# Optimization experiments

Hardware: AMD Instinct MI355X
Metric: run time of the kernel (lower is better)

## Reference

```python
import jax, jax.numpy as jnp
import numpy as np

D_MODEL = 1024
HEAD = 16
K_D = D_MODEL // HEAD
SEQ_LEN = 2048
BATCH = 4
NEG = 1e10


def setup_inputs() -> dict:
    key = jax.random.key(0)
    ks = jax.random.split(key, 5)
    x = jax.random.normal(ks[0], (BATCH, SEQ_LEN, D_MODEL), dtype=jnp.float32)
    # params (torch Linear stored as [out,in]; we store [in,out] and matmul directly)
    W_attn = jax.random.normal(ks[1], (D_MODEL, 3 * D_MODEL), dtype=jnp.float32) * 0.02
    b_attn = jnp.zeros((3 * D_MODEL,), dtype=jnp.float32)
    W_proj = jax.random.normal(ks[2], (D_MODEL, D_MODEL), dtype=jnp.float32) * 0.02
    b_proj = jnp.zeros((D_MODEL,), dtype=jnp.float32)
    return {"x": x, "W_attn": W_attn, "b_attn": b_attn, "W_proj": W_proj, "b_proj": b_proj}


def reference(x, W_attn, b_attn, W_proj, b_proj):
    B, S, D = x.shape
    qkv = x @ W_attn + b_attn                     # [B,S,3D]
    # NOTE: source splits as (value, query, key) in that order
    value, query, key = jnp.split(qkv, 3, axis=-1)

    def heads(t):  # [B,S,D] -> [B,H,S,k_d]
        return t.reshape(B, S, HEAD, K_D).transpose(0, 2, 1, 3)

    v, q, k = heads(value), heads(query), heads(key)
    present = jnp.stack((k, v))                   # [2,B,H,S,k_d]

    scores = jnp.einsum('bhqd,bhkd->bhqk', q, k) / jnp.sqrt(jnp.float32(K_D))
    bias = jnp.tril(jnp.ones((S, S), dtype=scores.dtype))[None, None]
    scores = scores * bias - NEG * (1.0 - bias)
    attn = jax.nn.softmax(scores, axis=-1)
    out = jnp.einsum('bhqk,bhkd->bhqd', attn, v)  # [B,H,S,k_d]
    out = out.transpose(0, 2, 1, 3).reshape(B, S, D)
    out = out @ W_proj + b_proj
    return out, present
```

## Files before the change

### kernel.cpp

```cpp
#include <hip/hip_runtime.h>

typedef __attribute__((ext_vector_type(8))) short short8;
typedef __attribute__((ext_vector_type(4))) short short4v;
typedef __attribute__((ext_vector_type(4))) float f32x4;
typedef __attribute__((ext_vector_type(16))) float f32x16;
typedef __attribute__((ext_vector_type(4))) unsigned int u32x4;
typedef __attribute__((ext_vector_type(2))) unsigned int u32x2;
typedef unsigned int u32;

#define D_MODEL 1024
#define HEADS 16
#define KD 64
#define SEQ 2048
#define BATCH 4
#define NTOK (BATCH*SEQ)
#define QKV_N (3*D_MODEL)

__device__ inline float bf2f(unsigned short u) {
    unsigned x = ((unsigned)u) << 16;
    return __builtin_bit_cast(float, x);
}
__device__ inline unsigned short f2bf(float f) {
    unsigned u = __builtin_bit_cast(unsigned, f);
    u += 0x7FFFu + ((u >> 16) & 1u);
    return (unsigned short)(u >> 16);
}
__device__ __forceinline__ void gload_lds16(const unsigned short* g, unsigned short* l) {
    __builtin_amdgcn_global_load_lds(
        (const __attribute__((address_space(1))) void*)g,
        (__attribute__((address_space(3))) void*)l, 16, 0, 0);
}
__device__ __forceinline__ u32 cvtpk(float lo, float hi) {
    u32 r; asm("v_cvt_pk_bf16_f32 %0, %1, %2" : "=v"(r) : "v"(lo), "v"(hi)); return r;
}
__device__ __forceinline__ void pl32swap(u32& a, u32& b) {
#if __has_builtin(__builtin_amdgcn_permlane32_swap)
    u32x2 r = __builtin_amdgcn_permlane32_swap(a, b, 0, 0);
    a = r[0]; b = r[1];
#else
    u32 pa = (u32)__shfl_xor((int)a, 32, 64);
    u32 pb = (u32)__shfl_xor((int)b, 32, 64);
    bool hb = (threadIdx.x & 32) != 0;
    u32 na = hb ? pb : a;
    u32 nb = hb ? b : pa;
    a = na; b = nb;
#endif
}
__device__ __forceinline__ float pairmax(float x) {
    u32 a = __builtin_bit_cast(u32, x), b = a;
    pl32swap(a, b);
    return fmaxf(x, fmaxf(__builtin_bit_cast(float, a), __builtin_bit_cast(float, b)));
}
__device__ __forceinline__ float pairsum(float x) {
    u32 a = __builtin_bit_cast(u32, x), b = a;
    pl32swap(a, b);
    return __builtin_bit_cast(float, a) + __builtin_bit_cast(float, b);
}

__global__ __launch_bounds__(256) void cvt_kernel(
    const float* __restrict__ x, unsigned short* __restrict__ y)
{
    size_t i = (size_t)blockIdx.x * 256 + threadIdx.x;
    f32x4 a = *reinterpret_cast<const f32x4*>(x + i*8);
    f32x4 b = *reinterpret_cast<const f32x4*>(x + i*8 + 4);
    short8 o;
    #pragma unroll
    for (int j = 0; j < 4; ++j) { o[j] = (short)f2bf(a[j]); o[j+4] = (short)f2bf(b[j]); }
    *reinterpret_cast<short8*>(y + i*8) = o;
}

__global__ __launch_bounds__(256) void transpose_kernel(
    const float* __restrict__ W, unsigned short* __restrict__ WT, int K, int N)
{
    __shared__ unsigned short T[64][80];
    const int tid = threadIdx.x;
    const int n0 = blockIdx.x * 64, k0 = blockIdx.y * 64;

    int r  = tid >> 2;
    int cq = tid & 3;
    const float* src = W + (size_t)(k0 + r) * N + n0 + cq*16;
    #pragma unroll
    for (int q = 0; q < 4; ++q) {
        f32x4 v = *reinterpret_cast<const f32x4*>(src + q*4);
        #pragma unroll
        for (int j = 0; j < 4; ++j) T[cq*16 + q*4 + j][r] = f2bf(v[j]);
    }
    __syncthreads();
    int c  = tid >> 2;
    int rq = tid & 3;
    short8 o0 = *reinterpret_cast<const short8*>(&T[c][rq*16]);
    short8 o1 = *reinterpret_cast<const short8*>(&T[c][rq*16 + 8]);
    unsigned short* dst = WT + (size_t)(n0 + c) * K + k0 + rq*16;
    *reinterpret_cast<short8*>(dst)     = o0;
    *reinterpret_cast<short8*>(dst + 8) = o1;
}

template<int Y_F32, int FUSE>
__global__ __launch_bounds__(256) void gemm_bt_kernel(
    const unsigned short* __restrict__ A, const unsigned short* __restrict__ BT,
    const float* __restrict__ bias, void* __restrict__ Yv,
    unsigned short* __restrict__ vtg, float* __restrict__ pres,
    int M, int N, int K)
{
    __shared__ unsigned short sA[2][128*64];
    __shared__ unsigned short sB[2][128*64];

    const int tid = threadIdx.x, lane = tid & 63, w = tid >> 6;
    const int l15 = lane & 15, lg = lane >> 4;

    const int nwg = gridDim.x * gridDim.y;
    const int bid = blockIdx.y * gridDim.x + blockIdx.x;
    const int swz = (bid & 7) * (nwg >> 3) + (bid >> 3);
    const int n0 = (swz % gridDim.x) * 128;
    const int m0 = (swz / gridDim.x) * 128;

    const int wr = w >> 1, wc = w & 1;

    f32x4 acc[4][4];
    #pragma unroll
    for (int m = 0; m < 4; ++m)
        #pragma unroll
        for (int n = 0; n < 4; ++n) acc[m][n] = f32x4{0,0,0,0};

    const int ldrow = (lane >> 3);
    const int slot  = lane & 7;
    const int nkt = K >> 6;

    #pragma unroll
    for (int i = 0; i < 4; ++i) {
        int kb  = w*4 + i;
        int row = kb*8 + ldrow;
        int sc  = slot ^ (row & 7);
        gload_lds16(&A [(size_t)(m0 + row) * K + sc*8], &sA[0][kb*512]);
        gload_lds16(&BT[(size_t)(n0 + row) * K + sc*8], &sB[0][kb*512]);
    }
    __syncthreads();

    for (int kt = 0; kt < nkt; ++kt) {
        const int buf = kt & 1;

        if (kt + 1 < nkt) {
            const int k1 = (kt + 1) << 6;
            #pragma unroll
            for (int i = 0; i < 4; ++i) {
                int kb  = w*4 + i;
                int row = kb*8 + ldrow;
                int sc  = slot ^ (row & 7);
                gload_lds16(&A [(size_t)(m0 + row) * K + k1 + sc*8], &sA[buf^1][kb*512]);
                gload_lds16(&BT[(size_t)(n0 + row) * K + k1 + sc*8], &sB[buf^1][kb*512]);
            }
        }

        #pragma unroll
        for (int kk = 0; kk < 2; ++kk) {
            short8 af[4], bfr[4];
            #pragma unroll
            for (int m = 0; m < 4; ++m) {
                int row = wr*64 + m*16 + l15;
                int ch  = (4*kk + lg) ^ (row & 7);
                af[m] = *reinterpret_cast<const short8*>(&sA[buf][row*64 + ch*8]);
            }
            #pragma unroll
            for (int n = 0; n < 4; ++n) {
                int row = wc*64 + n*16 + l15;
                int ch  = (4*kk + lg) ^ (row & 7);
                bfr[n] = *reinterpret_cast<const short8*>(&sB[buf][row*64 + ch*8]);
            }
            __builtin_amdgcn_s_setprio(1);
            #pragma unroll
            for (int m = 0; m < 4; ++m)
                #pragma unroll
                for (int n = 0; n < 4; ++n)
                    acc[m][n] = __builtin_amdgcn_mfma_f32_16x16x32_bf16(
                        af[m], bfr[n], acc[m][n], 0, 0, 0);
            __builtin_amdgcn_s_setprio(0);
        }
        __syncthreads();
    }

    #pragma unroll
    for (int n = 0; n < 4; ++n) {
        int col = n0 + wc*64 + n*16 + l15;
        float bv = bias[col];
        #pragma unroll
        for (int m = 0; m < 4; ++m) {
            int row0 = m0 + wr*64 + m*16 + lg*4;
            float v0 = acc[m][n][0] + bv;
            float v1 = acc[m][n][1] + bv;
            float v2 = acc[m][n][2] + bv;
            float v3 = acc[m][n][3] + bv;
            if (Y_F32) {
                float* Y = (float*)Yv;
                Y[(size_t)(row0+0) * N + col] = v0;
                Y[(size_t)(row0+1) * N + col] = v1;
                Y[(size_t)(row0+2) * N + col] = v2;
                Y[(size_t)(row0+3) * N + col] = v3;
            } else {
                unsigned short* Y = (unsigned short*)Yv;
                Y[(size_t)(row0+0) * N + col] = f2bf(v0);
                Y[(size_t)(row0+1) * N + col] = f2bf(v1);
                Y[(size_t)(row0+2) * N + col] = f2bf(v2);
                Y[(size_t)(row0+3) * N + col] = f2bf(v3);
            }
            if (FUSE && n0 < D_MODEL) {
                int hh = col >> 6, dd = col & 63;
                int bb = row0 >> 11, ss = row0 & (SEQ - 1);
                short4v pk;
                pk[0] = (short)f2bf(v0); pk[1] = (short)f2bf(v1);
                pk[2] = (short)f2bf(v2); pk[3] = (short)f2bf(v3);
                *reinterpret_cast<short4v*>(
                    vtg + (((size_t)bb*HEADS + hh)*KD + dd)*SEQ + ss) = pk;
                float* pv = pres + (size_t)BATCH*HEADS*SEQ*KD
                          + (((size_t)bb*HEADS + hh)*SEQ + ss)*KD + dd;
                pv[0] = v0; pv[KD] = v1; pv[2*KD] = v2; pv[3*KD] = v3;
            }
            if (FUSE && n0 >= 2*D_MODEL) {
                int rel = col - 2*D_MODEL;
                int hh = rel >> 6, dd = rel & 63;
                int bb = row0 >> 11, ss = row0 & (SEQ - 1);
                float* pk2 = pres + (((size_t)bb*HEADS + hh)*SEQ + ss)*KD + dd;
                pk2[0] = v0; pk2[KD] = v1; pk2[2*KD] = v2; pk2[3*KD] = v3;
            }
        }
    }
}

__global__ __launch_bounds__(256) void attn_kernel(
    const unsigned short* __restrict__ qkv,
    const unsigned short* __restrict__ vtg,
    unsigned short* __restrict__ aout)
{
    __shared__ unsigned short Kl[2][64*64];
    __shared__ unsigned short Vl[2][64*64];

    const int tid  = threadIdx.x;
    const int lane = tid & 63;
    const int w    = tid >> 6;
    const int l31  = lane & 31, hi = lane >> 5;

    const int bid = blockIdx.x;
    const int hb  = bid & 63;
    const int qb  = 15 - (bid >> 6);
    const int h = hb & 15, b = hb >> 4;

    const unsigned short* base  = qkv + (size_t)b * SEQ * QKV_N;
    const unsigned short* vbase = vtg + ((size_t)b * HEADS + h) * KD * SEQ;
    const int qoff = D_MODEL + h*KD;
    const int koff = 2*D_MODEL + h*KD;

    const float SCALE2 = 0.125f * 1.44269504088896f;
    const float THR_RAW = 44.36f;

    const int ldrow = lane >> 3;
    const int slot  = lane & 7;
    const int ksw   = l31 & 7;

    const int q0 = qb * 128;
    const int qrow  = q0 + w*32 + l31;
    const int qminw = q0 + w*32;

    short8 qf[4];
    #pragma unroll
    for (int ks = 0; ks < 4; ++ks)
        qf[ks] = *reinterpret_cast<const short8*>(
            base + (size_t)qrow * QKV_N + qoff + ks*16 + hi*8);

    f32x16 o0, o1;
    #pragma unroll
    for (int r = 0; r < 16; ++r) { o0[r] = 0.f; o1[r] = 0.f; }
    float m = -1e30f, msc = -1e30f * 0.180336887f, sr = 0.f;

    const int nt = 2*qb + 2;

    #pragma unroll
    for (int i = 0; i < 2; ++i) {
        int kb = w*2 + i, row = kb*8 + ldrow, sc = slot ^ (row & 7);
        gload_lds16(&base[(size_t)row * QKV_N + koff + sc*8], &Kl[0][kb*512]);
        gload_lds16(&vbase[(size_t)row * SEQ + sc*8],         &Vl[0][kb*512]);
    }
    __syncthreads();

    for (int t = 0; t < nt; ++t) {
        const int buf = t & 1;

        if (t + 1 < nt) {
            #pragma unroll
            for (int i = 0; i < 2; ++i) {
                int kb = w*2 + i, row = kb*8 + ldrow, sc = slot ^ (row & 7);
                gload_lds16(&base[(size_t)((t+1)*64 + row) * QKV_N + koff + sc*8],
                            &Kl[buf^1][kb*512]);
                gload_lds16(&vbase[(size_t)row * SEQ + (t+1)*64 + sc*8],
                            &Vl[buf^1][kb*512]);
            }
        }

        const int d0 = qminw - t*64;
        if (d0 > -32) {
            f32x16 sa, sb;
            #pragma unroll
            for (int r = 0; r < 16; ++r) { sa[r] = 0.f; sb[r] = 0.f; }
            __builtin_amdgcn_s_setprio(1);
            #pragma unroll
            for (int ks = 0; ks < 4; ++ks) {
                short8 kf = *reinterpret_cast<const short8*>(
                    &Kl[buf][l31*64 + ((2*ks + hi) ^ ksw)*8]);
                sa = __builtin_amdgcn_mfma_f32_32x32x16_bf16(kf, qf[ks], sa, 0, 0, 0);
            }
            #pragma unroll
            for (int ks = 0; ks < 4; ++ks) {
                short8 kf = *reinterpret_cast<const short8*>(
                    &Kl[buf][(32 + l31)*64 + ((2*ks + hi) ^ ksw)*8]);
                sb = __builtin_amdgcn_mfma_f32_32x32x16_bf16(kf, qf[ks], sb, 0, 0, 0);
            }
            __builtin_amdgcn_s_setprio(0);

            if (d0 <= 32) {
                const int kqA = l31 + d0      - 4*hi;
                const int kqB = l31 + d0 - 32 - 4*hi;
                #pragma unroll
                for (int r = 0; r < 16; ++r) {
                    const int cr = (r & 3) + 8*(r >> 2);
                    if (d0 == 0) sa[r] = (cr <= kqA) ? sa[r] : -1e30f;
                    sb[r] = (cr <= kqB) ? sb[r] : -1e30f;
                }
            }

            float x[8];
            #pragma unroll
            for (int i = 0; i < 8; ++i)
                x[i] = fmaxf(fmaxf(sa[2*i], sa[2*i+1]), fmaxf(sb[2*i], sb[2*i+1]));
            float pm = fmaxf(fmaxf(fmaxf(x[0], x[1]), fmaxf(x[2], x[3])),
                             fmaxf(fmaxf(x[4], x[5]), fmaxf(x[6], x[7])));
            pm = pairmax(pm);
            if (!__all(pm <= m + THR_RAW)) {
                float mn  = fmaxf(m, pm);
                float fac = exp2f((m - mn) * SCALE2);
                sr *= fac;
                #pragma unroll
                for (int r = 0; r < 16; ++r) { o0[r] *= fac; o1[r] *= fac; }
                m = mn; msc = m * SCALE2;
            }

            #pragma unroll
            for (int r = 0; r < 16; ++r) {
                sa[r] = exp2f(sa[r]*SCALE2 - msc);
                sb[r] = exp2f(sb[r]*SCALE2 - msc);
            }
            float u[8];
            #pragma unroll
            for (int i = 0; i < 8; ++i)
                u[i] = (sa[2*i] + sa[2*i+1]) + (sb[2*i] + sb[2*i+1]);
            float ts = ((u[0]+u[1]) + (u[2]+u[3])) + ((u[4]+u[5]) + (u[6]+u[7]));
            sr += pairsum(ts);

            u32 WA[8], WB[8];
            #pragma unroll
            for (int wi = 0; wi < 8; ++wi) {
                WA[wi] = cvtpk(sa[2*wi], sa[2*wi+1]);
                WB[wi] = cvtpk(sb[2*wi], sb[2*wi+1]);
            }

            #pragma unroll
            for (int h32 = 0; h32 < 2; ++h32) {
                #pragma unroll
                for (int ks = 0; ks < 2; ++ks) {
                    u32 W0 = h32 ? WB[4*ks+0] : WA[4*ks+0];
                    u32 W1 = h32 ? WB[4*ks+1] : WA[4*ks+1];
                    u32 W2 = h32 ? WB[4*ks+2] : WA[4*ks+2];
                    u32 W3 = h32 ? WB[4*ks+3] : WA[4*ks+3];
                    u32 s0 = hi ? W0 : W2;
                    u32 s1 = hi ? W1 : W3;
                    u32 r0 = (u32)__shfl_xor((int)s0, 32, 64);
                    u32 r1 = (u32)__shfl_xor((int)s1, 32, 64);
                    u32x4 wv;
                    wv[0] = hi ? r0 : W0;
                    wv[1] = hi ? r1 : W1;
                    wv[2] = hi ? W2 : r0;
                    wv[3] = hi ? W3 : r1;
                    short8 pfrag = __builtin_bit_cast(short8, wv);
                    __builtin_amdgcn_s_setprio(1);
                    #pragma unroll
                    for (int dt = 0; dt < 2; ++dt) {
                        short8 vf = *reinterpret_cast<const short8*>(
                            &Vl[buf][(dt*32 + l31)*64 + ((4*h32 + 2*ks + hi) ^ ksw)*8]);
                        if (dt == 0)
                            o0 = __builtin_amdgcn_mfma_f32_32x32x16_bf16(vf, pfrag, o0, 0, 0, 0);
                        else
                            o1 = __builtin_amdgcn_mfma_f32_32x32x16_bf16(vf, pfrag, o1, 0, 0, 0);
                    }
                    __builtin_amdgcn_s_setprio(0);
                }
            }
        }
        __syncthreads();
    }

    const float inv = 1.0f / sr;
    unsigned short* orow = aout + ((size_t)b * SEQ + qrow) * D_MODEL + h*KD;
    #pragma unroll
    for (int dt = 0; dt < 2; ++dt) {
        #pragma unroll
        for (int g = 0; g < 4; ++g) {
            short4v pk;
            #pragma unroll
            for (int j = 0; j < 4; ++j) {
                float v = (dt == 0 ? o0[4*g + j] : o1[4*g + j]) * inv;
                pk[j] = (short)f2bf(v);
            }
            *reinterpret_cast<short4v*>(orow + dt*32 + 8*g + 4*hi) = pk;
        }
    }
}

extern "C" void kernel_launch(void* const* d_in, const int* in_sizes, int n_in,
                              void* d_out, int out_size, void* d_ws, size_t ws_size,
                              hipStream_t stream)
{
    const float* x      = (const float*)d_in[0];
    const float* W_attn = (const float*)d_in[1];
    const float* b_attn = (const float*)d_in[2];
    const float* W_proj = (const float*)d_in[3];
    const float* b_proj = (const float*)d_in[4];
    float* out = (float*)d_out;

    unsigned short* qkv  = (unsigned short*)d_ws;
    unsigned short* xbf  = qkv + (size_t)NTOK * QKV_N;
    unsigned short* aout = xbf;
    unsigned short* WT   = xbf + (size_t)NTOK * D_MODEL;
    unsigned short* WpT  = WT + (size_t)QKV_N * D_MODEL;
    unsigned short* vtg  = WpT + (size_t)D_MODEL * D_MODEL;
    float* pres = out + (size_t)NTOK * D_MODEL;

    cvt_kernel<<<(NTOK * D_MODEL / 8) / 256, 256, 0, stream>>>(x, xbf);
    dim3 gt1(QKV_N / 64, D_MODEL / 64);
    transpose_kernel<<<gt1, 256, 0, stream>>>(W_attn, WT, D_MODEL, QKV_N);
    dim3 gt2(D_MODEL / 64, D_MODEL / 64);
    transpose_kernel<<<gt2, 256, 0, stream>>>(W_proj, WpT, D_MODEL, D_MODEL);

    dim3 g1(QKV_N / 128, NTOK / 128);
    gemm_bt_kernel<0, 1><<<g1, 256, 0, stream>>>(xbf, WT, b_attn, qkv, vtg, pres,
                                                 NTOK, QKV_N, D_MODEL);

    attn_kernel<<<1024, 256, 0, stream>>>(qkv, vtg, aout);

    dim3 g2(D_MODEL / 128, NTOK / 128);
    gemm_bt_kernel<1, 0><<<g2, 256, 0, stream>>>(aout, WpT, b_proj, out,
                                                 nullptr, nullptr,
                                                 NTOK, D_MODEL, D_MODEL);
}
```

Baseline: 210.5 us.

## Pair complementary causal query blocks per workgroup to share K/V tiles

Each attention workgroup now processes two query blocks, p and 15-p, so every block does equal causal work, and the grid halves. The K/V tiles loaded into LDS are reused for both query blocks while their ranges overlap, which cuts global and LDS load traffic per unit of work. The code is split into qk/softmax/pv helpers. Doubled accumulator and Q-fragment state raises register pressure, which may reduce occupancy.

```diff
diff --git a/kernel.cpp b/kernel.cpp
--- a/kernel.cpp
+++ b/kernel.cpp
@@ -55,6 +55,117 @@
     u32 a = __builtin_bit_cast(u32, x), b = a;
     pl32swap(a, b);
     return __builtin_bit_cast(float, a) + __builtin_bit_cast(float, b);
+}
+
+#define SCALE2f (0.125f * 1.44269504088896f)
+#define THR_RAWf 44.36f
+
+__device__ __forceinline__ void qk_tile(
+    const unsigned short* __restrict__ Klb, const short8 (&qf)[4],
+    int l31, int hi, int ksw, f32x16& sa, f32x16& sb)
+{
+    #pragma unroll
+    for (int r = 0; r < 16; ++r) { sa[r] = 0.f; sb[r] = 0.f; }
+    __builtin_amdgcn_s_setprio(1);
+    #pragma unroll
+    for (int ks = 0; ks < 4; ++ks) {
+        short8 kf = *reinterpret_cast<const short8*>(
+            &Klb[l31*64 + ((2*ks + hi) ^ ksw)*8]);
+        sa = __builtin_amdgcn_mfma_f32_32x32x16_bf16(kf, qf[ks], sa, 0, 0, 0);
+    }
+    #pragma unroll
+    for (int ks = 0; ks < 4; ++ks) {
+        short8 kf = *reinterpret_cast<const short8*>(
+            &Klb[(32 + l31)*64 + ((2*ks + hi) ^ ksw)*8]);
+        sb = __builtin_amdgcn_mfma_f32_32x32x16_bf16(kf, qf[ks], sb, 0, 0, 0);
+    }
+    __builtin_amdgcn_s_setprio(0);
+}
+
+template<bool MASK>
+__device__ __forceinline__ void sm_tile(
+    f32x16& sa, f32x16& sb, int d0, int l31, int hi,
+    float& m, float& msc, float& sr, f32x16& o0, f32x16& o1,
+    u32 (&WA)[8], u32 (&WB)[8])
+{
+    if (MASK && d0 <= 32) {
+        const int kqA = l31 + d0      - 4*hi;
+        const int kqB = l31 + d0 - 32 - 4*hi;
+        #pragma unroll
+        for (int r = 0; r < 16; ++r) {
+            const int cr = (r & 3) + 8*(r >> 2);
+            if (d0 == 0) sa[r] = (cr <= kqA) ? sa[r] : -1e30f;
+            sb[r] = (cr <= kqB) ? sb[r] : -1e30f;
+        }
+    }
+    float x[8];
+    #pragma unroll
+    for (int i = 0; i < 8; ++i)
+        x[i] = fmaxf(fmaxf(sa[2*i], sa[2*i+1]), fmaxf(sb[2*i], sb[2*i+1]));
+    float pm = fmaxf(fmaxf(fmaxf(x[0], x[1]), fmaxf(x[2], x[3])),
+                     fmaxf(fmaxf(x[4], x[5]), fmaxf(x[6], x[7])));
+    pm = pairmax(pm);
+    if (!__all(pm <= m + THR_RAWf)) {
+        float mn  = fmaxf(m, pm);
+        float fac = exp2f((m - mn) * SCALE2f);
+        sr *= fac;
+        #pragma unroll
+        for (int r = 0; r < 16; ++r) { o0[r] *= fac; o1[r] *= fac; }
+        m = mn; msc = m * SCALE2f;
+    }
+    #pragma unroll
+    for (int r = 0; r < 16; ++r) {
+        sa[r] = exp2f(sa[r]*SCALE2f - msc);
+        sb[r] = exp2f(sb[r]*SCALE2f - msc);
+    }
+    float u[8];
+    #pragma unroll
+    for (int i = 0; i < 8; ++i)
+        u[i] = (sa[2*i] + sa[2*i+1]) + (sb[2*i] + sb[2*i+1]);
+    float ts = ((u[0]+u[1]) + (u[2]+u[3])) + ((u[4]+u[5]) + (u[6]+u[7]));
+    sr += pairsum(ts);
+    #pragma unroll
+    for (int wi = 0; wi < 8; ++wi) {
+        WA[wi] = cvtpk(sa[2*wi], sa[2*wi+1]);
+        WB[wi] = cvtpk(sb[2*wi], sb[2*wi+1]);
+    }
+}
+
+__device__ __forceinline__ void pv_tile(
+    const unsigned short* __restrict__ Vlb, const u32 (&WA)[8], const u32 (&WB)[8],
+    int l31, int hi, int ksw, f32x16& o0, f32x16& o1)
+{
+    #pragma unroll
+    for (int h32 = 0; h32 < 2; ++h32) {
+        #pragma unroll
+        for (int ks = 0; ks < 2; ++ks) {
+            u32 W0 = h32 ? WB[4*ks+0] : WA[4*ks+0];
+            u32 W1 = h32 ? WB[4*ks+1] : WA[4*ks+1];
+            u32 W2 = h32 ? WB[4*ks+2] : WA[4*ks+2];
+            u32 W3 = h32 ? WB[4*ks+3] : WA[4*ks+3];
+            u32 s0 = hi ? W0 : W2;
+            u32 s1 = hi ? W1 : W3;
+            u32 r0 = (u32)__shfl_xor((int)s0, 32, 64);
+            u32 r1 = (u32)__shfl_xor((int)s1, 32, 64);
+            u32x4 wv;
+            wv[0] = hi ? r0 : W0;
+            wv[1] = hi ? r1 : W1;
+            wv[2] = hi ? W2 : r0;
+            wv[3] = hi ? W3 : r1;
+            short8 pfrag = __builtin_bit_cast(short8, wv);
+            __builtin_amdgcn_s_setprio(1);
+            #pragma unroll
+            for (int dt = 0; dt < 2; ++dt) {
+                short8 vf = *reinterpret_cast<const short8*>(
+                    &Vlb[(dt*32 + l31)*64 + ((4*h32 + 2*ks + hi) ^ ksw)*8]);
+                if (dt == 0)
+                    o0 = __builtin_amdgcn_mfma_f32_32x32x16_bf16(vf, pfrag, o0, 0, 0, 0);
+                else
+                    o1 = __builtin_amdgcn_mfma_f32_32x32x16_bf16(vf, pfrag, o1, 0, 0, 0);
+            }
+            __builtin_amdgcn_s_setprio(0);
+        }
+    }
 }
 
 __global__ __launch_bounds__(256) void cvt_kernel(
@@ -240,7 +351,7 @@
 
     const int bid = blockIdx.x;
     const int hb  = bid & 63;
-    const int qb  = 15 - (bid >> 6);
+    const int p   = bid >> 6;
     const int h = hb & 15, b = hb >> 4;
 
     const unsigned short* base  = qkv + (size_t)b * SEQ * QKV_N;
@@ -248,29 +359,32 @@
     const int qoff = D_MODEL + h*KD;
     const int koff = 2*D_MODEL + h*KD;
 
-    const float SCALE2 = 0.125f * 1.44269504088896f;
-    const float THR_RAW = 44.36f;
-
     const int ldrow = lane >> 3;
     const int slot  = lane & 7;
     const int ksw   = l31 & 7;
 
-    const int q0 = qb * 128;
-    const int qrow  = q0 + w*32 + l31;
-    const int qminw = q0 + w*32;
-
-    short8 qf[4];
-    #pragma unroll
-    for (int ks = 0; ks < 4; ++ks)
-        qf[ks] = *reinterpret_cast<const short8*>(
-            base + (size_t)qrow * QKV_N + qoff + ks*16 + hi*8);
-
-    f32x16 o0, o1;
-    #pragma unroll
-    for (int r = 0; r < 16; ++r) { o0[r] = 0.f; o1[r] = 0.f; }
-    float m = -1e30f, msc = -1e30f * 0.180336887f, sr = 0.f;
-
-    const int nt = 2*qb + 2;
+    const int qbA = p, qbB = 15 - p;
+    const int qminwA = qbA*128 + w*32;
+    const int qminwB = qbB*128 + w*32;
+    const int qrowA  = qminwA + l31;
+    const int qrowB  = qminwB + l31;
+
+    short8 qfA[4], qfB[4];
+    #pragma unroll
+    for (int ks = 0; ks < 4; ++ks) {
+        qfA[ks] = *reinterpret_cast<const short8*>(
+            base + (size_t)qrowA * QKV_N + qoff + ks*16 + hi*8);
+        qfB[ks] = *reinterpret_cast<const short8*>(
+            base + (size_t)qrowB * QKV_N + qoff + ks*16 + hi*8);
+    }
+
+    f32x16 o0A, o1A, o0B, o1B;
+    #pragma unroll
+    for (int r = 0; r < 16; ++r) { o0A[r]=0.f; o1A[r]=0.f; o0B[r]=0.f; o1B[r]=0.f; }
+    float mA = -1e30f, mscA = -1e30f * SCALE2f, srA = 0.f;
+    float mB = -1e30f, mscB = -1e30f * SCALE2f, srB = 0.f;
+
+    const int nt = 2*qbB + 2;
 
     #pragma unroll
     for (int i = 0; i < 2; ++i) {
@@ -294,120 +408,60 @@
             }
         }
 
-        const int d0 = qminw - t*64;
-        if (d0 > -32) {
-            f32x16 sa, sb;
-            #pragma unroll
-            for (int r = 0; r < 16; ++r) { sa[r] = 0.f; sb[r] = 0.f; }
-            __builtin_amdgcn_s_setprio(1);
-            #pragma unroll
-            for (int ks = 0; ks < 4; ++ks) {
-                short8 kf = *reinterpret_cast<const short8*>(
-                    &Kl[buf][l31*64 + ((2*ks + hi) ^ ksw)*8]);
-                sa = __builtin_amdgcn_mfma_f32_32x32x16_bf16(kf, qf[ks], sa, 0, 0, 0);
-            }
-            #pragma unroll
-            for (int ks = 0; ks < 4; ++ks) {
-                short8 kf = *reinterpret_cast<const short8*>(
-                    &Kl[buf][(32 + l31)*64 + ((2*ks + hi) ^ ksw)*8]);
-                sb = __builtin_amdgcn_mfma_f32_32x32x16_bf16(kf, qf[ks], sb, 0, 0, 0);
-            }
-            __builtin_amdgcn_s_setprio(0);
-
-            if (d0 <= 32) {
-                const int kqA = l31 + d0      - 4*hi;
-                const int kqB = l31 + d0 - 32 - 4*hi;
+        const int d0A = qminwA - t*64;
+        const int d0B = qminwB - t*64;
+
+        if (d0A > -32) {
+            f32x16 saA, sbA, saB, sbB;
+            qk_tile(Kl[buf], qfA, l31, hi, ksw, saA, sbA);
+            qk_tile(Kl[buf], qfB, l31, hi, ksw, saB, sbB);
+            u32 WAA[8], WBA[8], WAB[8], WBB[8];
+            sm_tile<true >(saA, sbA, d0A, l31, hi, mA, mscA, srA, o0A, o1A, WAA, WBA);
+            sm_tile<false>(saB, sbB, 0,   l31, hi, mB, mscB, srB, o0B, o1B, WAB, WBB);
+            pv_tile(Vl[buf], WAA, WBA, l31, hi, ksw, o0A, o1A);
+            pv_tile(Vl[buf], WAB, WBB, l31, hi, ksw, o0B, o1B);
+        } else if (d0B > -32) {
+            f32x16 saB, sbB;
+            qk_tile(Kl[buf], qfB, l31, hi, ksw, saB, sbB);
+            u32 WAB[8], WBB[8];
+            sm_tile<true >(saB, sbB, d0B, l31, hi, mB, mscB, srB, o0B, o1B, WAB, WBB);
+            pv_tile(Vl[buf], WAB, WBB, l31, hi, ksw, o0B, o1B);
+        }
+        __syncthreads();
+    }
+
+    {
+        const float inv = 1.0f / srA;
+        unsigned short* orow = aout + ((size_t)b * SEQ + qrowA) * D_MODEL + h*KD;
+        #pragma unroll
+        for (int dt = 0; dt < 2; ++dt) {
+            #pragma unroll
+            for (int g = 0; g < 4; ++g) {
+                short4v pk;
                 #pragma unroll
-                for (int r = 0; r < 16; ++r) {
-                    const int cr = (r & 3) + 8*(r >> 2);
-                    if (d0 == 0) sa[r] = (cr <= kqA) ? sa[r] : -1e30f;
-                    sb[r] = (cr <= kqB) ? sb[r] : -1e30f;
+                for (int j = 0; j < 4; ++j) {
+                    float v = (dt == 0 ? o0A[4*g + j] : o1A[4*g + j]) * inv;
+                    pk[j] = (short)f2bf(v);
                 }
-            }
-
-            float x[8];
-            #pragma unroll
-            for (int i = 0; i < 8; ++i)
-                x[i] = fmaxf(fmaxf(sa[2*i], sa[2*i+1]), fmaxf(sb[2*i], sb[2*i+1]));
-            float pm = fmaxf(fmaxf(fmaxf(x[0], x[1]), fmaxf(x[2], x[3])),
-                             fmaxf(fmaxf(x[4], x[5]), fmaxf(x[6], x[7])));
-            pm = pairmax(pm);
-            if (!__all(pm <= m + THR_RAW)) {
-                float mn  = fmaxf(m, pm);
-                float fac = exp2f((m - mn) * SCALE2);
-                sr *= fac;
+                *reinterpret_cast<short4v*>(orow + dt*32 + 8*g + 4*hi) = pk;
+            }
+        }
+    }
+    {
+        const float inv = 1.0f / srB;
+        unsigned short* orow = aout + ((size_t)b * SEQ + qrowB) * D_MODEL + h*KD;
+        #pragma unroll
+        for (int dt = 0; dt < 2; ++dt) {
+            #pragma unroll
+            for (int g = 0; g < 4; ++g) {
+                short4v pk;
                 #pragma unroll
-                for (int r = 0; r < 16; ++r) { o0[r] *= fac; o1[r] *= fac; }
-                m = mn; msc = m * SCALE2;
-            }
-
-            #pragma unroll
-            for (int r = 0; r < 16; ++r) {
-                sa[r] = exp2f(sa[r]*SCALE2 - msc);
-                sb[r] = exp2f(sb[r]*SCALE2 - msc);
-            }
-            float u[8];
-            #pragma unroll
-            for (int i = 0; i < 8; ++i)
-                u[i] = (sa[2*i] + sa[2*i+1]) + (sb[2*i] + sb[2*i+1]);
-            float ts = ((u[0]+u[1]) + (u[2]+u[3])) + ((u[4]+u[5]) + (u[6]+u[7]));
-            sr += pairsum(ts);
-
-            u32 WA[8], WB[8];
-            #pragma unroll
-            for (int wi = 0; wi < 8; ++wi) {
-                WA[wi] = cvtpk(sa[2*wi], sa[2*wi+1]);
-                WB[wi] = cvtpk(sb[2*wi], sb[2*wi+1]);
-            }
-
-            #pragma unroll
-            for (int h32 = 0; h32 < 2; ++h32) {
-                #pragma unroll
-                for (int ks = 0; ks < 2; ++ks) {
-                    u32 W0 = h32 ? WB[4*ks+0] : WA[4*ks+0];
-                    u32 W1 = h32 ? WB[4*ks+1] : WA[4*ks+1];
-                    u32 W2 = h32 ? WB[4*ks+2] : WA[4*ks+2];
-                    u32 W3 = h32 ? WB[4*ks+3] : WA[4*ks+3];
-                    u32 s0 = hi ? W0 : W2;
-                    u32 s1 = hi ? W1 : W3;
-                    u32 r0 = (u32)__shfl_xor((int)s0, 32, 64);
-                    u32 r1 = (u32)__shfl_xor((int)s1, 32, 64);
-                    u32x4 wv;
-                    wv[0] = hi ? r0 : W0;
-                    wv[1] = hi ? r1 : W1;
-                    wv[2] = hi ? W2 : r0;
-                    wv[3] = hi ? W3 : r1;
-                    short8 pfrag = __builtin_bit_cast(short8, wv);
-                    __builtin_amdgcn_s_setprio(1);
-                    #pragma unroll
-                    for (int dt = 0; dt < 2; ++dt) {
-                        short8 vf = *reinterpret_cast<const short8*>(
-                            &Vl[buf][(dt*32 + l31)*64 + ((4*h32 + 2*ks + hi) ^ ksw)*8]);
-                        if (dt == 0)
-                            o0 = __builtin_amdgcn_mfma_f32_32x32x16_bf16(vf, pfrag, o0, 0, 0, 0);
-                        else
-                            o1 = __builtin_amdgcn_mfma_f32_32x32x16_bf16(vf, pfrag, o1, 0, 0, 0);
-                    }
-                    __builtin_amdgcn_s_setprio(0);
+                for (int j = 0; j < 4; ++j) {
+                    float v = (dt == 0 ? o0B[4*g + j] : o1B[4*g + j]) * inv;
+                    pk[j] = (short)f2bf(v);
                 }
-            }
-        }
-        __syncthreads();
-    }
-
-    const float inv = 1.0f / sr;
-    unsigned short* orow = aout + ((size_t)b * SEQ + qrow) * D_MODEL + h*KD;
-    #pragma unroll
-    for (int dt = 0; dt < 2; ++dt) {
-        #pragma unroll
-        for (int g = 0; g < 4; ++g) {
-            short4v pk;
-            #pragma unroll
-            for (int j = 0; j < 4; ++j) {
-                float v = (dt == 0 ? o0[4*g + j] : o1[4*g + j]) * inv;
-                pk[j] = (short)f2bf(v);
-            }
-            *reinterpret_cast<short4v*>(orow + dt*32 + 8*g + 4*hi) = pk;
+                *reinterpret_cast<short4v*>(orow + dt*32 + 8*g + 4*hi) = pk;
+            }
         }
     }
 }
@@ -441,7 +495,7 @@
     gemm_bt_kernel<0, 1><<<g1, 256, 0, stream>>>(xbf, WT, b_attn, qkv, vtg, pres,
                                                  NTOK, QKV_N, D_MODEL);
 
-    attn_kernel<<<1024, 256, 0, stream>>>(qkv, vtg, aout);
+    attn_kernel<<<512, 256, 0, stream>>>(qkv, vtg, aout);
 
     dim3 g2(D_MODEL / 128, NTOK / 128);
     gemm_bt_kernel<1, 0><<<g2, 256, 0, stream>>>(aout, WpT, b_proj, out,
```

Result: slower. 255.9 us (+21.6%).

## Merge two adjacent query blocks into one 512-thread attention workgroup sharing K/V tiles

Applied to the files above, without the earlier changes.

The attention kernel now runs 512 threads per block, and two 4-wave groups handle adjacent 128-row query blocks (2i and 2i+1) of the same head. The K/V tiles are loaded into LDS once per block and shared by both groups, halving redundant global K/V traffic. The loop runs to the longer causal range (4i+4 tiles), so the lower query group idles through its final tiles. The change also halves the grid, and the bigger blocks may reduce occupancy and load balance.

```diff
diff --git a/kernel.cpp b/kernel.cpp
--- a/kernel.cpp
+++ b/kernel.cpp
@@ -225,7 +225,7 @@
     }
 }
 
-__global__ __launch_bounds__(256) void attn_kernel(
+__global__ __launch_bounds__(512) void attn_kernel(
     const unsigned short* __restrict__ qkv,
     const unsigned short* __restrict__ vtg,
     unsigned short* __restrict__ aout)
@@ -236,11 +236,14 @@
     const int tid  = threadIdx.x;
     const int lane = tid & 63;
     const int w    = tid >> 6;
+    const int wg   = w >> 2;
+    const int wl   = w & 3;
     const int l31  = lane & 31, hi = lane >> 5;
 
     const int bid = blockIdx.x;
     const int hb  = bid & 63;
-    const int qb  = 15 - (bid >> 6);
+    const int i   = 7 - (bid >> 6);
+    const int qb  = 2*i + wg;
     const int h = hb & 15, b = hb >> 4;
 
     const unsigned short* base  = qkv + (size_t)b * SEQ * QKV_N;
@@ -256,8 +259,8 @@
     const int ksw   = l31 & 7;
 
     const int q0 = qb * 128;
-    const int qrow  = q0 + w*32 + l31;
-    const int qminw = q0 + w*32;
+    const int qrow  = q0 + wl*32 + l31;
+    const int qminw = q0 + wl*32;
 
     short8 qf[4];
     #pragma unroll
@@ -270,13 +273,12 @@
     for (int r = 0; r < 16; ++r) { o0[r] = 0.f; o1[r] = 0.f; }
     float m = -1e30f, msc = -1e30f * 0.180336887f, sr = 0.f;
 
-    const int nt = 2*qb + 2;
-
-    #pragma unroll
-    for (int i = 0; i < 2; ++i) {
-        int kb = w*2 + i, row = kb*8 + ldrow, sc = slot ^ (row & 7);
-        gload_lds16(&base[(size_t)row * QKV_N + koff + sc*8], &Kl[0][kb*512]);
-        gload_lds16(&vbase[(size_t)row * SEQ + sc*8],         &Vl[0][kb*512]);
+    const int nt = 4*i + 4;
+
+    {
+        int row = w*8 + ldrow, sc = slot ^ (row & 7);
+        gload_lds16(&base[(size_t)row * QKV_N + koff + sc*8], &Kl[0][w*512]);
+        gload_lds16(&vbase[(size_t)row * SEQ + sc*8],         &Vl[0][w*512]);
     }
     __syncthreads();
 
@@ -284,14 +286,11 @@
         const int buf = t & 1;
 
         if (t + 1 < nt) {
-            #pragma unroll
-            for (int i = 0; i < 2; ++i) {
-                int kb = w*2 + i, row = kb*8 + ldrow, sc = slot ^ (row & 7);
-                gload_lds16(&base[(size_t)((t+1)*64 + row) * QKV_N + koff + sc*8],
-                            &Kl[buf^1][kb*512]);
-                gload_lds16(&vbase[(size_t)row * SEQ + (t+1)*64 + sc*8],
-                            &Vl[buf^1][kb*512]);
-            }
+            int row = w*8 + ldrow, sc = slot ^ (row & 7);
+            gload_lds16(&base[(size_t)((t+1)*64 + row) * QKV_N + koff + sc*8],
+                        &Kl[buf^1][w*512]);
+            gload_lds16(&vbase[(size_t)row * SEQ + (t+1)*64 + sc*8],
+                        &Vl[buf^1][w*512]);
         }
 
         const int d0 = qminw - t*64;
@@ -327,8 +326,8 @@
 
             float x[8];
             #pragma unroll
-            for (int i = 0; i < 8; ++i)
-                x[i] = fmaxf(fmaxf(sa[2*i], sa[2*i+1]), fmaxf(sb[2*i], sb[2*i+1]));
+            for (int ii = 0; ii < 8; ++ii)
+                x[ii] = fmaxf(fmaxf(sa[2*ii], sa[2*ii+1]), fmaxf(sb[2*ii], sb[2*ii+1]));
             float pm = fmaxf(fmaxf(fmaxf(x[0], x[1]), fmaxf(x[2], x[3])),
                              fmaxf(fmaxf(x[4], x[5]), fmaxf(x[6], x[7])));
             pm = pairmax(pm);
@@ -348,8 +347,8 @@
             }
             float u[8];
             #pragma unroll
-            for (int i = 0; i < 8; ++i)
-                u[i] = (sa[2*i] + sa[2*i+1]) + (sb[2*i] + sb[2*i+1]);
+            for (int ii = 0; ii < 8; ++ii)
+                u[ii] = (sa[2*ii] + sa[2*ii+1]) + (sb[2*ii] + sb[2*ii+1]);
             float ts = ((u[0]+u[1]) + (u[2]+u[3])) + ((u[4]+u[5]) + (u[6]+u[7]));
             sr += pairsum(ts);
 
@@ -441,7 +440,7 @@
     gemm_bt_kernel<0, 1><<<g1, 256, 0, stream>>>(xbf, WT, b_attn, qkv, vtg, pres,
                                                  NTOK, QKV_N, D_MODEL);
 
-    attn_kernel<<<1024, 256, 0, stream>>>(qkv, vtg, aout);
+    attn_kernel<<<512, 512, 0, stream>>>(qkv, vtg, aout);
 
     dim3 g2(D_MODEL / 128, NTOK / 128);
     gemm_bt_kernel<1, 0><<<g2, 256, 0, stream>>>(aout, WpT, b_proj, out,
```

Measured after the change: 201.8 us. 4.2% less time.
